# Performance work log

Measured on AMD Instinct MI355X. Metric: run time of the kernel, lower is better.

Reference implementation:

```python
import jax, jax.numpy as jnp
import numpy as np

TEMPERATURE = 0.6
REPETITION_PENALTY = 1.2
VOCAB = 50257


def setup_inputs() -> dict:
    key = jax.random.key(0)
    k1, k2 = jax.random.split(key)
    logits = jax.random.normal(k1, (8, 64, VOCAB), dtype=jnp.float32)
    prev_tokens = jax.random.randint(k2, (64, 200), 0, VOCAB, dtype=jnp.int64)
    return {"logits": logits, "prev_tokens": prev_tokens}


def reference(logits, prev_tokens):
    # logits: [B, S, V]; prev_tokens: [S, P] token ids previously generated per sequence.
    B, S, V = logits.shape
    # set-semantics mask of penalized (seq, token) pairs; duplicate ids collapse to one.
    mask = jnp.zeros((S, V), dtype=bool).at[
        jnp.arange(S)[:, None], prev_tokens
    ].set(True)  # [S, V]
    # torch.all over dim 0: penalty multiplies if all batch logits negative, else divides.
    all_neg = jnp.all(logits < 0, axis=0, keepdims=True)  # [1, S, V]
    penalized = jnp.where(all_neg, logits * REPETITION_PENALTY, logits / REPETITION_PENALTY)
    logits = jnp.where(mask[None, :, :], penalized, logits)
    # Categorical(logits=x) -> probs = softmax(x); temperature scaling fused.
    return jax.nn.softmax(logits / TEMPERATURE, axis=-1)
```

## Files before the change

### kernel.cpp

```cpp
#include <hip/hip_runtime.h>
#include <math.h>

#define BB 8
#define SS 64
#define VV 50257
#define PP 200
#define NMASK 1571
#define NT 1024
#define ITER 13
constexpr float RP   = 1.2f;
constexpr float TINV = 1.0f / 0.6f;

typedef float f32x4 __attribute__((ext_vector_type(4)));

__global__ __launch_bounds__(NT, 4) void sch_fused_kernel(
        const float* __restrict__ logits,
        const int*   __restrict__ prev,
        float*       __restrict__ out) {
    __shared__ unsigned mask[NMASK];
    __shared__ float ss[16];
    __shared__ float bc_li;

    const int bs  = blockIdx.x;
    const int s   = bs & (SS - 1);
    const int tid = threadIdx.x;
    const float* row  = logits + (size_t)bs * VV;
    float*       orow = out    + (size_t)bs * VV;

    const int a0   = (4 - (bs & 3)) & 3;
    const int nb   = (VV - a0) >> 2;
    const int tail = VV - a0 - (nb << 2);
    const int tstart = a0 + (nb << 2);

    const f32x4* body = (const f32x4*)(row + a0);
    f32x4 buf[ITER];
    #pragma unroll
    for (int k = 0; k < ITER; ++k) {
        int i = tid + k * NT;
        if (i < nb) buf[k] = body[i];
    }
    float xscal = 0.0f;
    const bool has_head = (tid < a0);
    const bool has_tail = (tid >= 4 && tid < 4 + tail);
    if (has_head) xscal = row[tid];
    if (has_tail) xscal = row[tstart + tid - 4];

    int   vtok = -1;
    float lv[BB];
    if (tid < PP) {
        vtok = prev[s * PP + tid];
        #pragma unroll
        for (int b = 0; b < BB; ++b)
            lv[b] = logits[((size_t)(b * SS + s)) * VV + vtok];
    }
    for (int i = tid; i < NMASK; i += NT) mask[i] = 0u;
    __syncthreads();

    float delta  = 0.0f;
    float eadj   = 0.0f;
    bool  winner = false;
    if (tid < PP) {
        unsigned bit = 1u << (vtok & 31);
        unsigned old = atomicOr(&mask[vtok >> 5], bit);
        winner = (old & bit) == 0u;
        if (winner) {
            bool all_neg = true;
            #pragma unroll
            for (int b = 0; b < BB; ++b) all_neg = all_neg && (lv[b] < 0.0f);
            const float myraw = lv[bs >> 6];
            const float adj   = all_neg ? myraw * RP : myraw / RP;
            eadj  = __expf(adj * TINV);
            delta = eadj - __expf(myraw * TINV);
        }
    }

    float escal = (has_head || has_tail) ? __expf(xscal * TINV) : 0.0f;
    float accx = 0.f, accy = 0.f, accz = 0.f, accw = 0.f;
    #pragma unroll
    for (int k = 0; k < ITER; ++k) {
        int i = tid + k * NT;
        if (i < nb) {
            f32x4 x = buf[k];
            f32x4 e;
            e.x = __expf(x.x * TINV);
            e.y = __expf(x.y * TINV);
            e.z = __expf(x.z * TINV);
            e.w = __expf(x.w * TINV);
            buf[k] = e;
            accx += e.x; accy += e.y; accz += e.z; accw += e.w;
        }
    }
    float sum = (accx + accy) + (accz + accw) + escal + delta;

    #pragma unroll
    for (int off = 1; off < 64; off <<= 1)
        sum += __shfl_xor(sum, off);
    const int wave = tid >> 6, lane = tid & 63;
    if (lane == 0) ss[wave] = sum;
    __syncthreads();
    if (tid == 0) {
        float S0 = ss[0];
        #pragma unroll
        for (int w = 1; w < 16; ++w) S0 += ss[w];
        bc_li = 1.0f / S0;
    }
    __syncthreads();
    const float li = bc_li;

    f32x4* obody = (f32x4*)(orow + a0);
    #pragma unroll
    for (int k = 0; k < ITER; ++k) {
        int i = tid + k * NT;
        if (i < nb) {
            f32x4 e = buf[k];
            f32x4 o;
            o.x = e.x * li; o.y = e.y * li; o.z = e.z * li; o.w = e.w * li;
            __builtin_nontemporal_store(o, &obody[i]);
        }
    }
    if (has_head) __builtin_nontemporal_store(escal * li, &orow[tid]);
    if (has_tail) __builtin_nontemporal_store(escal * li, &orow[tstart + tid - 4]);

    __syncthreads();
    if (winner) orow[vtok] = eadj * li;
}

extern "C" void kernel_launch(void* const* d_in, const int* in_sizes, int n_in,
                              void* d_out, int out_size, void* d_ws, size_t ws_size,
                              hipStream_t stream) {
    const float* logits = (const float*)d_in[0];
    const int*   prev   = (const int*)d_in[1];
    float* out = (float*)d_out;

    sch_fused_kernel<<<BB * SS, NT, 0, stream>>>(logits, prev, out);
}
```

Measured before the change: 194.8 us.

## Recompute exponentials in second pass instead of holding row in registers

The kernel no longer keeps the 13 float4 values per thread in registers between the sum pass and the write pass. It re-reads the row from global memory (likely served by cache) and recomputes exp in the output pass, and it drops the occupancy hint from launch bounds. This lowers register pressure at the cost of a second read of the logits and doubled exp work. The up-front load of the whole row, which overlapped with the mask setup, is also removed.

```diff
diff --git a/kernel.cpp b/kernel.cpp
--- a/kernel.cpp
+++ b/kernel.cpp
@@ -13,7 +13,7 @@
 
 typedef float f32x4 __attribute__((ext_vector_type(4)));
 
-__global__ __launch_bounds__(NT, 4) void sch_fused_kernel(
+__global__ __launch_bounds__(NT) void sch_fused_kernel(
         const float* __restrict__ logits,
         const int*   __restrict__ prev,
         float*       __restrict__ out) {
@@ -31,19 +31,9 @@
     const int nb   = (VV - a0) >> 2;
     const int tail = VV - a0 - (nb << 2);
     const int tstart = a0 + (nb << 2);
-
     const f32x4* body = (const f32x4*)(row + a0);
-    f32x4 buf[ITER];
-    #pragma unroll
-    for (int k = 0; k < ITER; ++k) {
-        int i = tid + k * NT;
-        if (i < nb) buf[k] = body[i];
-    }
-    float xscal = 0.0f;
     const bool has_head = (tid < a0);
     const bool has_tail = (tid >= 4 && tid < 4 + tail);
-    if (has_head) xscal = row[tid];
-    if (has_tail) xscal = row[tstart + tid - 4];
 
     int   vtok = -1;
     float lv[BB];
@@ -56,41 +46,39 @@
     for (int i = tid; i < NMASK; i += NT) mask[i] = 0u;
     __syncthreads();
 
-    float delta  = 0.0f;
-    float eadj   = 0.0f;
-    bool  winner = false;
+    bool winner = false;
     if (tid < PP) {
         unsigned bit = 1u << (vtok & 31);
         unsigned old = atomicOr(&mask[vtok >> 5], bit);
         winner = (old & bit) == 0u;
-        if (winner) {
-            bool all_neg = true;
-            #pragma unroll
-            for (int b = 0; b < BB; ++b) all_neg = all_neg && (lv[b] < 0.0f);
-            const float myraw = lv[bs >> 6];
-            const float adj   = all_neg ? myraw * RP : myraw / RP;
-            eadj  = __expf(adj * TINV);
-            delta = eadj - __expf(myraw * TINV);
-        }
     }
 
-    float escal = (has_head || has_tail) ? __expf(xscal * TINV) : 0.0f;
     float accx = 0.f, accy = 0.f, accz = 0.f, accw = 0.f;
     #pragma unroll
     for (int k = 0; k < ITER; ++k) {
         int i = tid + k * NT;
         if (i < nb) {
-            f32x4 x = buf[k];
-            f32x4 e;
-            e.x = __expf(x.x * TINV);
-            e.y = __expf(x.y * TINV);
-            e.z = __expf(x.z * TINV);
-            e.w = __expf(x.w * TINV);
-            buf[k] = e;
-            accx += e.x; accy += e.y; accz += e.z; accw += e.w;
+            f32x4 x = body[i];
+            accx += __expf(x.x * TINV);
+            accy += __expf(x.y * TINV);
+            accz += __expf(x.z * TINV);
+            accw += __expf(x.w * TINV);
         }
     }
-    float sum = (accx + accy) + (accz + accw) + escal + delta;
+    float sum = (accx + accy) + (accz + accw);
+    if (has_head) sum += __expf(row[tid] * TINV);
+    if (has_tail) sum += __expf(row[tstart + tid - 4] * TINV);
+
+    float eadj = 0.0f;
+    if (winner) {
+        bool all_neg = true;
+        #pragma unroll
+        for (int b = 0; b < BB; ++b) all_neg = all_neg && (lv[b] < 0.0f);
+        const float myraw = lv[bs >> 6];
+        const float adj   = all_neg ? myraw * RP : myraw / RP;
+        eadj = __expf(adj * TINV);
+        sum += eadj - __expf(myraw * TINV);
+    }
 
     #pragma unroll
     for (int off = 1; off < 64; off <<= 1)
@@ -112,14 +100,20 @@
     for (int k = 0; k < ITER; ++k) {
         int i = tid + k * NT;
         if (i < nb) {
-            f32x4 e = buf[k];
+            f32x4 x = body[i];
             f32x4 o;
-            o.x = e.x * li; o.y = e.y * li; o.z = e.z * li; o.w = e.w * li;
+            o.x = __expf(x.x * TINV) * li;
+            o.y = __expf(x.y * TINV) * li;
+            o.z = __expf(x.z * TINV) * li;
+            o.w = __expf(x.w * TINV) * li;
             __builtin_nontemporal_store(o, &obody[i]);
         }
     }
-    if (has_head) __builtin_nontemporal_store(escal * li, &orow[tid]);
-    if (has_tail) __builtin_nontemporal_store(escal * li, &orow[tstart + tid - 4]);
+    if (has_head)
+        __builtin_nontemporal_store(__expf(row[tid] * TINV) * li, &orow[tid]);
+    if (has_tail)
+        __builtin_nontemporal_store(__expf(row[tstart + tid - 4] * TINV) * li,
+                                    &orow[tstart + tid - 4]);
 
     __syncthreads();
     if (winner) orow[vtok] = eadj * li;
```

Result: slower. 202.8 us (+4.1%).
